# Kernel tuning notes

Measured on AMD Instinct MI355X. Metric: run time of the kernel, lower is better.

Reference implementation:

```python
import jax, jax.numpy as jnp
import numpy as np

IN_FEATURES = 4096
OUT_FEATURES = 4096  # % 16 == 0, so pad_out = 0
BATCH, SEQ = 4, 2048


def setup_inputs() -> dict:
    key = jax.random.key(0)
    k_x, k_w, k_b = jax.random.split(key, 3)
    # int8 activations and weights (W8A8)
    x = jax.random.randint(k_x, (BATCH, SEQ, IN_FEATURES), -128, 128, dtype=jnp.int32).astype(jnp.int8)
    # weight stored as (in_features, out_features), matching qlinear.weight layout
    weight = jax.random.randint(k_w, (IN_FEATURES, OUT_FEATURES), -128, 128, dtype=jnp.int32).astype(jnp.int8)
    # a: scalar input scale; b: per-output-channel dequant/requant scale
    a = jnp.full((1, 1), 0.0123, dtype=jnp.float32)
    b = jax.random.uniform(k_b, (1, OUT_FEATURES), dtype=jnp.float32, minval=0.001, maxval=0.02)
    return {"x": x, "weight": weight, "a": a, "b": b}


def reference(x, weight, a, b):
    # x: [B, S, K] int8; weight: [K, N] int8; a: [1,1] f32; b: [1,N] f32
    x_shape = x.shape
    x2d = x.reshape(-1, x_shape[-1])
    acc = jnp.matmul(x2d, weight, preferred_element_type=jnp.int32)
    # fused dequant (scalar a) + per-channel requant (b), round-to-nearest, saturate to int8
    y_f = acc.astype(jnp.float32) * a * b  # [T, N]
    y = jnp.clip(jnp.round(y_f), -128.0, 127.0).astype(jnp.int8)
    return y.reshape(*x_shape[:-1], -1)
```

## Files before the change

### kernel.cpp

```cpp
#include <hip/hip_runtime.h>
#include <stdint.h>

#define M_DIM 8192
#define N_DIM 4096
#define K_DIM 4096
#define BM 128
#define BN 128
#define BK 64

typedef int v4i __attribute__((ext_vector_type(4)));
typedef int v16i __attribute__((ext_vector_type(16)));
typedef unsigned u32;

__device__ __forceinline__ void gll16(const void* g, void* l) {
  __builtin_amdgcn_global_load_lds(
      (const __attribute__((address_space(1))) void*)g,
      (__attribute__((address_space(3))) void*)l, 16, 0, 0);
}

__device__ __forceinline__ u32 pack4(const int4 v) {
  return (v.x & 0xffu) | ((v.y & 0xffu) << 8) | ((v.z & 0xffu) << 16) |
         ((u32)(v.w & 0xffu) << 24);
}

__device__ __forceinline__ bool hdr_is_i32(const int* __restrict__ X, int tid,
                                           int* ok) {
  if (tid == 0) *ok = 1;
  __syncthreads();
  int good = 1;
  for (int i = tid; i < 1024; i += 256) {
    const int w = X[i];
    good &= (w == (int)(int8_t)(w & 0xff));
  }
  if (!good) atomicAnd(ok, 0);
  __syncthreads();
  return *ok != 0;
}

__global__ __launch_bounds__(256) void detect_i32(const int* __restrict__ X,
                                                  u32* __restrict__ flag) {
  __shared__ int ok;
  const bool i32 = hdr_is_i32(X, threadIdx.x, &ok);
  if (threadIdx.x == 0) *flag = i32 ? 1u : 0u;
}

__global__ __launch_bounds__(256) void pack_x_f(const void* __restrict__ Xin,
                                                u32* __restrict__ out) {
  __shared__ int ok;
  const bool i32 = hdr_is_i32((const int*)Xin, threadIdx.x, &ok);
  const int base = blockIdx.x * 1024 + threadIdx.x;
  if (i32) {
    const int4* in = (const int4*)Xin;
#pragma unroll
    for (int j = 0; j < 4; ++j) {
      const int idx = base + j * 256;
      out[idx] = pack4(in[idx]);
    }
  } else {
    const u32* in = (const u32*)Xin;
#pragma unroll
    for (int j = 0; j < 4; ++j) {
      const int idx = base + j * 256;
      out[idx] = in[idx];
    }
  }
}

__global__ __launch_bounds__(256) void packT_w_f(const void* __restrict__ Wv,
                                                 int8_t* __restrict__ WT,
                                                 const int* __restrict__ Xhdr) {
  __shared__ u32 lds[64 * 21];
  __shared__ int ok;
  const int tid = threadIdx.x;
  const bool i32 = hdr_is_i32(Xhdr, tid, &ok);
  const int tk = blockIdx.x & 63;
  const int tn = blockIdx.x >> 6;
  const int k0 = tk * 64, n0 = tn * 64;

#pragma unroll
  for (int j = 0; j < 4; ++j) {
    const int id = j * 256 + tid;
    const int k = id >> 4, c = id & 15;
    u32 word;
    if (i32) {
      const int4 v =
          *(const int4*)((const int*)Wv + (size_t)(k0 + k) * N_DIM + n0 + c * 4);
      word = pack4(v);
    } else {
      word = *(const u32*)((const int8_t*)Wv + (size_t)(k0 + k) * N_DIM + n0 +
                           c * 4);
    }
    lds[k * 21 + c] = word;
  }
  __syncthreads();
  const int kd = tid & 15, nq = tid >> 4;
  const u32 d0 = lds[(kd * 4 + 0) * 21 + nq];
  const u32 d1 = lds[(kd * 4 + 1) * 21 + nq];
  const u32 d2 = lds[(kd * 4 + 2) * 21 + nq];
  const u32 d3 = lds[(kd * 4 + 3) * 21 + nq];
  u32* outp = (u32*)WT;
#pragma unroll
  for (int i = 0; i < 4; ++i) {
    const u32 e = ((d0 >> (8 * i)) & 0xffu) | (((d1 >> (8 * i)) & 0xffu) << 8) |
                  (((d2 >> (8 * i)) & 0xffu) << 16) |
                  (((d3 >> (8 * i)) & 0xffu) << 24);
    const int n = n0 + nq * 4 + i;
    outp[(size_t)n * (K_DIM / 4) + (k0 / 4) + kd] = e;
  }
}

__device__ __forceinline__ void epilogue(const v4i acc[4][4], float a,
                                         const float* __restrict__ bScale,
                                         int* __restrict__ Y, int bm, int bn,
                                         int wm, int wn, int quad, int l16) {
  const int nBase = bn * BN + wn * 64 + l16;
  float bs[4];
#pragma unroll
  for (int ni = 0; ni < 4; ++ni) bs[ni] = bScale[nBase + ni * 16];
#pragma unroll
  for (int mi = 0; mi < 4; ++mi) {
    const int m0 = bm * BM + wm * 64 + mi * 16 + quad * 4;
#pragma unroll
    for (int r = 0; r < 4; ++r) {
      int* row = Y + (size_t)(m0 + r) * N_DIM + nBase;
#pragma unroll
      for (int ni = 0; ni < 4; ++ni) {
        float v = ((float)acc[mi][ni][r] * a) * bs[ni];
        v = rintf(v);
        v = fminf(fmaxf(v, -128.f), 127.f);
        row[ni * 16] = (int)v;
      }
    }
  }
}

__global__ __launch_bounds__(512, 2) void gemm_256(
    const int8_t* __restrict__ X, const int8_t* __restrict__ WT,
    const float* __restrict__ aScale, const float* __restrict__ bScale,
    int* __restrict__ Y) {
  __shared__ __align__(16) int8_t lds[131072];
  const int tid = threadIdx.x;
  const int lane = tid & 63;
  const int wave = tid >> 6;
  const int l31 = lane & 31, h = lane >> 5;
  const int wm = wave >> 2, wn = wave & 3;

  const int swzb = (blockIdx.x & 7) * 64 + (blockIdx.x >> 3);
  const int bn = swzb & 15, bm = swzb >> 4;

  const int clog = (((tid & 3) ^ ((tid >> 3) & 3)) << 4);
  const int sw = (l31 >> 1) & 3;
  const int pc0 = (h ^ sw) << 4;
  const int pc1 = pc0 ^ 32;

  const int8_t* xa = X + (size_t)(bm * 256 + (tid >> 2)) * K_DIM + clog;
  const int8_t* xb = WT + (size_t)(bn * 256 + (tid >> 2)) * K_DIM + clog;
  int8_t* ldsA = lds + tid * 16;
  int8_t* ldsB = lds + 65536 + tid * 16;
  const int8_t* aB0 = lds + (wm * 128 + l31) * 64 + pc0;
  const int8_t* aB1 = lds + (wm * 128 + l31) * 64 + pc1;
  const int8_t* bB0 = lds + 65536 + (wn * 64 + l31) * 64 + pc0;
  const int8_t* bB1 = lds + 65536 + (wn * 64 + l31) * 64 + pc1;

  v16i acc[4][2] = {};

#pragma unroll
  for (int t = 0; t < 3; ++t) {
    gll16(xa + t * 64, ldsA + t * 16384);
    gll16(xa + (size_t)128 * K_DIM + t * 64, ldsA + t * 16384 + 8192);
    gll16(xb + t * 64, ldsB + t * 16384);
    gll16(xb + (size_t)128 * K_DIM + t * 64, ldsB + t * 16384 + 8192);
  }
  asm volatile("s_waitcnt vmcnt(8)" ::: "memory");
  __builtin_amdgcn_s_barrier();

  for (int g = 0; g < 64; ++g) {
    const int soff = (g & 3) << 14;
    const int poff = ((g + 3) & 3) << 14;
    const bool pre = g <= 60;
    v4i af[4], bf[2];
#pragma unroll
    for (int mi = 0; mi < 4; ++mi)
      af[mi] = *(const v4i*)(aB0 + soff + mi * 2048);
#pragma unroll
    for (int ni = 0; ni < 2; ++ni)
      bf[ni] = *(const v4i*)(bB0 + soff + ni * 2048);
    if (pre) {
      const int8_t* s = xa + (size_t)(g + 3) * 64;
      gll16(s, ldsA + poff);
      gll16(s + (size_t)128 * K_DIM, ldsA + poff + 8192);
    }
    __builtin_amdgcn_s_barrier();
    asm volatile("s_waitcnt lgkmcnt(0)" ::: "memory");
    __builtin_amdgcn_sched_barrier(0);
    __builtin_amdgcn_s_setprio(1);
#pragma unroll
    for (int mi = 0; mi < 4; ++mi)
#pragma unroll
      for (int ni = 0; ni < 2; ++ni)
        acc[mi][ni] = __builtin_amdgcn_mfma_i32_32x32x32_i8(
            af[mi], bf[ni], acc[mi][ni], 0, 0, 0);
    __builtin_amdgcn_s_setprio(0);
    __builtin_amdgcn_s_barrier();

#pragma unroll
    for (int mi = 0; mi < 4; ++mi)
      af[mi] = *(const v4i*)(aB1 + soff + mi * 2048);
#pragma unroll
    for (int ni = 0; ni < 2; ++ni)
      bf[ni] = *(const v4i*)(bB1 + soff + ni * 2048);
    if (pre) {
      const int8_t* s = xb + (size_t)(g + 3) * 64;
      gll16(s, ldsB + poff);
      gll16(s + (size_t)128 * K_DIM, ldsB + poff + 8192);
    }
    __builtin_amdgcn_s_barrier();
    asm volatile("s_waitcnt lgkmcnt(0)" ::: "memory");
    __builtin_amdgcn_sched_barrier(0);
    __builtin_amdgcn_s_setprio(1);
#pragma unroll
    for (int mi = 0; mi < 4; ++mi)
#pragma unroll
      for (int ni = 0; ni < 2; ++ni)
        acc[mi][ni] = __builtin_amdgcn_mfma_i32_32x32x32_i8(
            af[mi], bf[ni], acc[mi][ni], 0, 0, 0);
    __builtin_amdgcn_s_setprio(0);
    if (g < 61)
      asm volatile("s_waitcnt vmcnt(8)" ::: "memory");
    else if (g == 61)
      asm volatile("s_waitcnt vmcnt(4)" ::: "memory");
    else
      asm volatile("s_waitcnt vmcnt(0)" ::: "memory");
    __builtin_amdgcn_s_barrier();
  }

  const float a = aScale[0];
  const int nB = bn * 256 + wn * 64 + l31;
  const float bs0 = bScale[nB];
  const float bs1 = bScale[nB + 32];
#pragma unroll
  for (int mi = 0; mi < 4; ++mi) {
#pragma unroll
    for (int ni = 0; ni < 2; ++ni) {
      const float bsv = ni ? bs1 : bs0;
      const int nCol = nB + ni * 32;
#pragma unroll
      for (int r = 0; r < 16; ++r) {
        const int row =
            bm * 256 + wm * 128 + mi * 32 + (r & 3) + 8 * (r >> 2) + 4 * h;
        float v = ((float)acc[mi][ni][r] * a) * bsv;
        v = rintf(v);
        v = fminf(fmaxf(v, -128.f), 127.f);
        Y[(size_t)row * N_DIM + nCol] = (int)v;
      }
    }
  }
}

__global__ __launch_bounds__(256) void gemm_inA(
    const void* __restrict__ Xv, const int8_t* __restrict__ WT,
    const float* __restrict__ aScale, const float* __restrict__ bScale,
    int* __restrict__ Y, const u32* __restrict__ flag) {
  __shared__ __align__(16) int8_t As[BM * BK];
  __shared__ __align__(16) int8_t Bs[BN * BK];
  const bool i32 = (*flag != 0);
  const int tid = threadIdx.x;
  const int lane = tid & 63, wave = tid >> 6;
  const int quad = lane >> 4, l16 = lane & 15;
  const int wm = wave & 1, wn = wave >> 1;
  const int bn = blockIdx.x & 31;
  const int bm = blockIdx.x >> 5;

  const int r0 = tid >> 2;
  const int c0 = (tid & 3) * 16;
  const int8_t* Bg0 = WT + (size_t)(bn * BN + r0) * K_DIM + c0;
  const int8_t* Bg1 = Bg0 + (size_t)64 * K_DIM;
  int8_t* Al0 = As + tid * 16;
  int8_t* Al1 = Al0 + 4096;
  int8_t* Bl0 = Bs + tid * 16;
  int8_t* Bl1 = Bl0 + 4096;

  v4i acc[4][4] = {};
  const int8_t* aLds = As + (wm * 64 + l16) * BK + quad * 16;
  const int8_t* bLds = Bs + (wn * 64 + l16) * BK + quad * 16;

  if (i32) {
    const int* Xg0 = (const int*)Xv + (size_t)(bm * BM + r0) * K_DIM + c0;
    const int* Xg1 = Xg0 + (size_t)64 * K_DIM;
    for (int k0 = 0; k0 < K_DIM; k0 += BK) {
      gll16(Bg0 + k0, Bl0);
      gll16(Bg1 + k0, Bl1);
      const int4* p0 = (const int4*)(Xg0 + k0);
      const int4* p1 = (const int4*)(Xg1 + k0);
      uint4 w0, w1;
      w0.x = pack4(p0[0]); w0.y = pack4(p0[1]);
      w0.z = pack4(p0[2]); w0.w = pack4(p0[3]);
      w1.x = pack4(p1[0]); w1.y = pack4(p1[1]);
      w1.z = pack4(p1[2]); w1.w = pack4(p1[3]);
      *(uint4*)Al0 = w0;
      *(uint4*)Al1 = w1;
      __syncthreads();
      v4i af[4], bf[4];
#pragma unroll
      for (int i = 0; i < 4; ++i) af[i] = *(const v4i*)(aLds + i * 16 * BK);
#pragma unroll
      for (int i = 0; i < 4; ++i) bf[i] = *(const v4i*)(bLds + i * 16 * BK);
#pragma unroll
      for (int mi = 0; mi < 4; ++mi)
#pragma unroll
        for (int ni = 0; ni < 4; ++ni)
          acc[mi][ni] = __builtin_amdgcn_mfma_i32_16x16x64_i8(
              af[mi], bf[ni], acc[mi][ni], 0, 0, 0);
      __syncthreads();
    }
  } else {
    const int8_t* Ag0 = (const int8_t*)Xv + (size_t)(bm * BM + r0) * K_DIM + c0;
    const int8_t* Ag1 = Ag0 + (size_t)64 * K_DIM;
    for (int k0 = 0; k0 < K_DIM; k0 += BK) {
      gll16(Ag0 + k0, Al0);
      gll16(Ag1 + k0, Al1);
      gll16(Bg0 + k0, Bl0);
      gll16(Bg1 + k0, Bl1);
      __syncthreads();
      v4i af[4], bf[4];
#pragma unroll
      for (int i = 0; i < 4; ++i) af[i] = *(const v4i*)(aLds + i * 16 * BK);
#pragma unroll
      for (int i = 0; i < 4; ++i) bf[i] = *(const v4i*)(bLds + i * 16 * BK);
#pragma unroll
      for (int mi = 0; mi < 4; ++mi)
#pragma unroll
        for (int ni = 0; ni < 4; ++ni)
          acc[mi][ni] = __builtin_amdgcn_mfma_i32_16x16x64_i8(
              af[mi], bf[ni], acc[mi][ni], 0, 0, 0);
      __syncthreads();
    }
  }
  epilogue(acc, aScale[0], bScale, Y, bm, bn, wm, wn, quad, l16);
}

extern "C" void kernel_launch(void* const* d_in, const int* in_sizes, int n_in,
                              void* d_out, int out_size, void* d_ws,
                              size_t ws_size, hipStream_t stream) {
  const void* Xv = d_in[0];
  const void* Wv = d_in[1];
  const float* a = (const float*)d_in[2];
  const float* b = (const float*)d_in[3];
  int* Y = (int*)d_out;

  const size_t xB = (size_t)M_DIM * K_DIM;
  const size_t wB = (size_t)N_DIM * K_DIM;

  if (ws_size >= xB + wB + 64) {
    int8_t* Xp = (int8_t*)d_ws;
    int8_t* WT = (int8_t*)d_ws + xB;
    pack_x_f<<<(M_DIM * K_DIM / 4) / 1024, 256, 0, stream>>>(Xv, (u32*)Xp);
    packT_w_f<<<(K_DIM / 64) * (N_DIM / 64), 256, 0, stream>>>(Wv, WT,
                                                               (const int*)Xv);
    gemm_256<<<(M_DIM / 256) * (N_DIM / 256), 512, 0, stream>>>(Xp, WT, a, b,
                                                                Y);
  } else if (ws_size >= wB + 64) {
    int8_t* WT = (int8_t*)d_ws;
    u32* flag = (u32*)((int8_t*)d_ws + wB);
    detect_i32<<<1, 256, 0, stream>>>((const int*)Xv, flag);
    packT_w_f<<<(K_DIM / 64) * (N_DIM / 64), 256, 0, stream>>>(Wv, WT,
                                                               (const int*)Xv);
    gemm_inA<<<(M_DIM / BM) * (N_DIM / BN), 256, 0, stream>>>(Xv, WT, a, b, Y,
                                                              flag);
  } else {
    int8_t* WT = (int8_t*)d_ws;
    u32* flag = (u32*)((int8_t*)d_ws + (ws_size >= wB + 4 ? wB : 0));
    detect_i32<<<1, 256, 0, stream>>>((const int*)Xv, flag);
    packT_w_f<<<(K_DIM / 64) * (N_DIM / 64), 256, 0, stream>>>(Wv, WT,
                                                               (const int*)Xv);
    gemm_inA<<<(M_DIM / BM) * (N_DIM / BN), 256, 0, stream>>>(Xv, WT, a, b, Y,
                                                              flag);
  }
}
```

Before: 438.2 us.

## Switch 256x256 GEMM to 16x16x64 int8 MFMA and simplify per-stage barriers

Replaces the 32x32x32 int8 MFMA tiles with 16x16x64 int8 MFMAs covering the full BK=64 in one instruction. The loop body now issues all A and B prefetches at the top of each k-step and drops the two intermediate barrier and lgkmcnt wait pairs, leaving one barrier per iteration. The epilogue is remapped to the 16x16 accumulator layout. This aims to cut barrier and synchronisation overhead and use a different MFMA shape. It raises accumulator count per wave and relies on the compiler to insert the LDS waits that were previously explicit.

```diff
diff --git a/kernel.cpp b/kernel.cpp
--- a/kernel.cpp
+++ b/kernel.cpp
@@ -9,7 +9,6 @@
 #define BK 64
 
 typedef int v4i __attribute__((ext_vector_type(4)));
-typedef int v16i __attribute__((ext_vector_type(16)));
 typedef unsigned u32;
 
 __device__ __forceinline__ void gll16(const void* g, void* l) {
@@ -142,27 +141,23 @@
   const int tid = threadIdx.x;
   const int lane = tid & 63;
   const int wave = tid >> 6;
-  const int l31 = lane & 31, h = lane >> 5;
+  const int quad = lane >> 4, l16 = lane & 15;
   const int wm = wave >> 2, wn = wave & 3;
 
   const int swzb = (blockIdx.x & 7) * 64 + (blockIdx.x >> 3);
   const int bn = swzb & 15, bm = swzb >> 4;
 
   const int clog = (((tid & 3) ^ ((tid >> 3) & 3)) << 4);
-  const int sw = (l31 >> 1) & 3;
-  const int pc0 = (h ^ sw) << 4;
-  const int pc1 = pc0 ^ 32;
+  const int pc = quad ^ ((l16 >> 1) & 3);
 
   const int8_t* xa = X + (size_t)(bm * 256 + (tid >> 2)) * K_DIM + clog;
   const int8_t* xb = WT + (size_t)(bn * 256 + (tid >> 2)) * K_DIM + clog;
   int8_t* ldsA = lds + tid * 16;
   int8_t* ldsB = lds + 65536 + tid * 16;
-  const int8_t* aB0 = lds + (wm * 128 + l31) * 64 + pc0;
-  const int8_t* aB1 = lds + (wm * 128 + l31) * 64 + pc1;
-  const int8_t* bB0 = lds + 65536 + (wn * 64 + l31) * 64 + pc0;
-  const int8_t* bB1 = lds + 65536 + (wn * 64 + l31) * 64 + pc1;
-
-  v16i acc[4][2] = {};
+  const int8_t* aBase = lds + (wm * 128 + l16) * 64 + pc * 16;
+  const int8_t* bBase = lds + 65536 + (wn * 64 + l16) * 64 + pc * 16;
+
+  v4i acc[8][4] = {};
 
 #pragma unroll
   for (int t = 0; t < 3; ++t) {
@@ -177,55 +172,37 @@
   for (int g = 0; g < 64; ++g) {
     const int soff = (g & 3) << 14;
     const int poff = ((g + 3) & 3) << 14;
-    const bool pre = g <= 60;
-    v4i af[4], bf[2];
+    if (g <= 60) {
+      const int8_t* sa = xa + (size_t)(g + 3) * 64;
+      const int8_t* sb = xb + (size_t)(g + 3) * 64;
+      gll16(sa, ldsA + poff);
+      gll16(sa + (size_t)128 * K_DIM, ldsA + poff + 8192);
+      gll16(sb, ldsB + poff);
+      gll16(sb + (size_t)128 * K_DIM, ldsB + poff + 8192);
+    }
+    v4i bf[4], af[4], ag[4];
+#pragma unroll
+    for (int i = 0; i < 4; ++i) bf[i] = *(const v4i*)(bBase + soff + i * 1024);
+#pragma unroll
+    for (int i = 0; i < 4; ++i) af[i] = *(const v4i*)(aBase + soff + i * 1024);
+    __builtin_amdgcn_s_setprio(1);
 #pragma unroll
     for (int mi = 0; mi < 4; ++mi)
-      af[mi] = *(const v4i*)(aB0 + soff + mi * 2048);
-#pragma unroll
-    for (int ni = 0; ni < 2; ++ni)
-      bf[ni] = *(const v4i*)(bB0 + soff + ni * 2048);
-    if (pre) {
-      const int8_t* s = xa + (size_t)(g + 3) * 64;
-      gll16(s, ldsA + poff);
-      gll16(s + (size_t)128 * K_DIM, ldsA + poff + 8192);
-    }
-    __builtin_amdgcn_s_barrier();
-    asm volatile("s_waitcnt lgkmcnt(0)" ::: "memory");
-    __builtin_amdgcn_sched_barrier(0);
-    __builtin_amdgcn_s_setprio(1);
+#pragma unroll
+      for (int ni = 0; ni < 4; ++ni)
+        acc[mi][ni] = __builtin_amdgcn_mfma_i32_16x16x64_i8(
+            af[mi], bf[ni], acc[mi][ni], 0, 0, 0);
+#pragma unroll
+    for (int i = 0; i < 4; ++i)
+      ag[i] = *(const v4i*)(aBase + soff + 4096 + i * 1024);
 #pragma unroll
     for (int mi = 0; mi < 4; ++mi)
 #pragma unroll
-      for (int ni = 0; ni < 2; ++ni)
-        acc[mi][ni] = __builtin_amdgcn_mfma_i32_32x32x32_i8(
-            af[mi], bf[ni], acc[mi][ni], 0, 0, 0);
+      for (int ni = 0; ni < 4; ++ni)
+        acc[4 + mi][ni] = __builtin_amdgcn_mfma_i32_16x16x64_i8(
+            ag[mi], bf[ni], acc[4 + mi][ni], 0, 0, 0);
     __builtin_amdgcn_s_setprio(0);
-    __builtin_amdgcn_s_barrier();
-
-#pragma unroll
-    for (int mi = 0; mi < 4; ++mi)
-      af[mi] = *(const v4i*)(aB1 + soff + mi * 2048);
-#pragma unroll
-    for (int ni = 0; ni < 2; ++ni)
-      bf[ni] = *(const v4i*)(bB1 + soff + ni * 2048);
-    if (pre) {
-      const int8_t* s = xb + (size_t)(g + 3) * 64;
-      gll16(s, ldsB + poff);
-      gll16(s + (size_t)128 * K_DIM, ldsB + poff + 8192);
-    }
-    __builtin_amdgcn_s_barrier();
-    asm volatile("s_waitcnt lgkmcnt(0)" ::: "memory");
-    __builtin_amdgcn_sched_barrier(0);
-    __builtin_amdgcn_s_setprio(1);
-#pragma unroll
-    for (int mi = 0; mi < 4; ++mi)
-#pragma unroll
-      for (int ni = 0; ni < 2; ++ni)
-        acc[mi][ni] = __builtin_amdgcn_mfma_i32_32x32x32_i8(
-            af[mi], bf[ni], acc[mi][ni], 0, 0, 0);
-    __builtin_amdgcn_s_setprio(0);
-    if (g < 61)
+    if (g <= 60)
       asm volatile("s_waitcnt vmcnt(8)" ::: "memory");
     else if (g == 61)
       asm volatile("s_waitcnt vmcnt(4)" ::: "memory");
@@ -235,23 +212,22 @@
   }
 
   const float a = aScale[0];
-  const int nB = bn * 256 + wn * 64 + l31;
-  const float bs0 = bScale[nB];
-  const float bs1 = bScale[nB + 32];
-#pragma unroll
-  for (int mi = 0; mi < 4; ++mi) {
-#pragma unroll
-    for (int ni = 0; ni < 2; ++ni) {
-      const float bsv = ni ? bs1 : bs0;
-      const int nCol = nB + ni * 32;
-#pragma unroll
-      for (int r = 0; r < 16; ++r) {
-        const int row =
-            bm * 256 + wm * 128 + mi * 32 + (r & 3) + 8 * (r >> 2) + 4 * h;
-        float v = ((float)acc[mi][ni][r] * a) * bsv;
+  const int nBase = bn * 256 + wn * 64 + l16;
+  float bs[4];
+#pragma unroll
+  for (int ni = 0; ni < 4; ++ni) bs[ni] = bScale[nBase + ni * 16];
+#pragma unroll
+  for (int mi = 0; mi < 8; ++mi) {
+    const int m0 = bm * 256 + wm * 128 + mi * 16 + quad * 4;
+#pragma unroll
+    for (int r = 0; r < 4; ++r) {
+      int* row = Y + (size_t)(m0 + r) * N_DIM + nBase;
+#pragma unroll
+      for (int ni = 0; ni < 4; ++ni) {
+        float v = ((float)acc[mi][ni][r] * a) * bs[ni];
         v = rintf(v);
         v = fminf(fmaxf(v, -128.f), 127.f);
-        Y[(size_t)row * N_DIM + nCol] = (int)v;
+        row[ni * 16] = (int)v;
       }
     }
   }
```

Result: faster. 407.1 us (-7.1%).
